# Kernel tuning notes

Measured on AMD Instinct MI355X. Metric: run time of the kernel, lower is better.

Reference implementation:

```python
import jax, jax.numpy as jnp
import numpy as np

L, CH, S = 4096, 512, 64
SAMPLE_RATE = 4096.0


def setup_inputs() -> dict:
    key = jax.random.key(0)
    kx, ka, kc = jax.random.split(key, 3)
    x = jax.random.normal(kx, (L, CH), dtype=jnp.float32)
    # original init: lognegA = log(arange(1..S)) broadcast over channels; any real values work
    lognegA = jnp.broadcast_to(jnp.log(jnp.arange(1, S + 1, dtype=jnp.float32)), (CH, S)) \
        + 0.0 * jax.random.normal(ka, (CH, S), dtype=jnp.float32)
    B = jnp.ones((CH, S), dtype=jnp.float32)
    C = 0.01 * jax.random.normal(kc, (CH, S), dtype=jnp.float32)  # nn.initializers.normal() stddev=0.01
    return {"x": x, "lognegA": lognegA, "B": B, "C": C}


def reference(x, lognegA, B, C):
    length = x.shape[0]
    dt = 1.0 / SAMPLE_RATE
    A = -jnp.exp(lognegA)                         # [C, S], strictly negative
    Bd = (jnp.exp(A * dt) - 1.0) * B / A          # discretized B, [C, S]
    # Vandermonde-style kernel: Ak[l, c, s] = exp(l * A[c, s] * dt)
    Ak = jnp.exp(jnp.einsum('l,cs->lcs', jnp.arange(length, dtype=x.dtype), A * dt))
    K = jnp.einsum('cs,lcs->lc', C * Bd, Ak)      # [L, C] per-channel kernel
    # per-channel full causal convolution, truncated to length
    y = jax.vmap(jnp.convolve, in_axes=1, out_axes=1)(x, K)[:length]
    return y
```

## Files before the change

kernel.cpp:

```cpp
#include <hip/hip_runtime.h>


namespace {

constexpr int L_ = 4096;
constexpr int CH_ = 512;
constexpr int S_ = 64;
constexpr float DT = 1.0f / 4096.0f;
constexpr int SC = S_ * CH_;
constexpr int SG = 16;
constexpr int T_ = 64;
constexpr int NC_ = L_ / T_;
constexpr int GJ = 16;
constexpr int NJ = NC_ / GJ;

__device__ __forceinline__ void params16(const float* __restrict__ la,
                                         const float* __restrict__ Bg,
                                         const float* __restrict__ Cg,
                                         int c, int s0, float* r, float* w) {
  const float4* lap = reinterpret_cast<const float4*>(la + c * S_ + s0);
  if (w == nullptr) {
#pragma unroll
    for (int q = 0; q < 4; ++q) {
      const float4 v = lap[q];
      const float a[4] = {v.x, v.y, v.z, v.w};
#pragma unroll
      for (int t = 0; t < 4; ++t) {
        const float A = -expf(a[t]);
        r[q * 4 + t] = expf(A * DT);
      }
    }
  } else {
    const float4* bp = reinterpret_cast<const float4*>(Bg + c * S_ + s0);
    const float4* cp = reinterpret_cast<const float4*>(Cg + c * S_ + s0);
#pragma unroll
    for (int q = 0; q < 4; ++q) {
      const float4 v = lap[q], bb = bp[q], cc = cp[q];
      const float a[4] = {v.x, v.y, v.z, v.w};
      const float bv[4] = {bb.x, bb.y, bb.z, bb.w};
      const float cv[4] = {cc.x, cc.y, cc.z, cc.w};
#pragma unroll
      for (int t = 0; t < 4; ++t) {
        const float A = -expf(a[t]);
        const float rr = expf(A * DT);
        r[q * 4 + t] = rr;
        w[q * 4 + t] = cv[t] * ((rr - 1.0f) * bv[t] / A);
      }
    }
  }
}

__global__ __launch_bounds__(256)
void k_local(const float* __restrict__ x, const float* __restrict__ la,
             float* __restrict__ E) {
  const int lane = threadIdx.x & 63;
  const int g = threadIdx.x >> 6;
  const int k = blockIdx.x >> 3;
  const int c = ((blockIdx.x & 7) << 6) + lane;
  const int s0 = g * SG;

  const float* xp = x + (size_t)k * T_ * CH_ + c;
  float xb[16];
#pragma unroll
  for (int j = 0; j < 16; ++j) xb[j] = xp[j * CH_];

  float r[SG], h[SG];
  params16(la, nullptr, nullptr, c, s0, r, nullptr);
#pragma unroll
  for (int i = 0; i < SG; ++i) h[i] = 0.0f;

  for (int l0 = 0; l0 < T_; l0 += 16) {
    float xc[16];
#pragma unroll
    for (int j = 0; j < 16; ++j) xc[j] = xb[j];
    const int ln = (l0 + 16 < T_) ? l0 + 16 : l0;
#pragma unroll
    for (int j = 0; j < 16; ++j) xb[j] = xp[(ln + j) * CH_];
#pragma unroll
    for (int j = 0; j < 16; ++j) {
      const float xv = xc[j];
#pragma unroll
      for (int i = 0; i < SG; ++i) h[i] = fmaf(r[i], h[i], xv);
    }
  }

  float* ew = E + (size_t)k * SC + s0 * CH_ + c;
#pragma unroll
  for (int i = 0; i < SG; ++i) ew[i * CH_] = h[i];
}

__global__ __launch_bounds__(256)
void k_comb(const float* __restrict__ la, float* __restrict__ carry) {
  __shared__ float aggs[NJ][64];
  const int p = threadIdx.x & 63;
  const int j = threadIdx.x >> 6;
  const int pid = (blockIdx.x << 6) + p;
  const int s = pid >> 9;
  const int c = pid & (CH_ - 1);

  float v[GJ];
#pragma unroll
  for (int m = 0; m < GJ; ++m) v[m] = carry[(size_t)(j * GJ + m) * SC + pid];

  const float A = -expf(la[c * S_ + s]);
  const float rT = expf(A * (DT * (float)T_));
  float rTG = rT;
  rTG *= rTG;
  rTG *= rTG;
  rTG *= rTG;
  rTG *= rTG;

  float agg = 0.0f;
#pragma unroll
  for (int m = 0; m < GJ; ++m) agg = fmaf(rT, agg, v[m]);
  aggs[j][p] = agg;
  __syncthreads();

  float G = 0.0f;
  for (int j2 = 0; j2 < j; ++j2) G = fmaf(rTG, G, aggs[j2][p]);

  float st = G;
#pragma unroll
  for (int m = 0; m < GJ; ++m) {
    carry[(size_t)(j * GJ + m) * SC + pid] = st;
    st = fmaf(rT, st, v[m]);
  }
}

template <int T, bool USE_CARRY>
__global__ __launch_bounds__(256)
void k_scan(const float* __restrict__ x, const float* __restrict__ la,
            const float* __restrict__ Bg, const float* __restrict__ Cg,
            const float* __restrict__ carry, float* __restrict__ y) {
  __shared__ float lds[4][8][64];

  const int lane = threadIdx.x & 63;
  const int g = threadIdx.x >> 6;
  const int k = blockIdx.x >> 3;
  const int cb = (blockIdx.x & 7) << 6;
  const int c = cb + lane;
  const int s0 = g * SG;

  float h[SG];
  if (USE_CARRY) {
    const float* crd = carry + (size_t)k * SC + s0 * CH_ + c;
#pragma unroll
    for (int i = 0; i < SG; ++i) h[i] = crd[i * CH_];
  } else {
#pragma unroll
    for (int i = 0; i < SG; ++i) h[i] = 0.0f;
  }
  const float* xp = x + (size_t)k * T * CH_ + c;
  float xb[8];
#pragma unroll
  for (int j = 0; j < 8; ++j) xb[j] = xp[j * CH_];

  float r[SG], w[SG];
  params16(la, Bg, Cg, c, s0, r, w);

  float* yp = y + (size_t)k * T * CH_;

  for (int l = 0; l < T; l += 8) {
    float xc[8];
#pragma unroll
    for (int j = 0; j < 8; ++j) xc[j] = xb[j];
    const int ln = (l + 8 < T) ? l + 8 : l;
#pragma unroll
    for (int j = 0; j < 8; ++j) xb[j] = xp[(ln + j) * CH_];

    float part[8];
#pragma unroll
    for (int jj = 0; jj < 8; ++jj) {
      const float xv = xc[jj];
      float a0 = 0, a1 = 0, a2 = 0, a3 = 0;
#pragma unroll
      for (int i = 0; i < SG; i += 4) {
        h[i]     = fmaf(r[i],     h[i],     xv);
        h[i + 1] = fmaf(r[i + 1], h[i + 1], xv);
        h[i + 2] = fmaf(r[i + 2], h[i + 2], xv);
        h[i + 3] = fmaf(r[i + 3], h[i + 3], xv);
        a0 = fmaf(w[i],     h[i],     a0);
        a1 = fmaf(w[i + 1], h[i + 1], a1);
        a2 = fmaf(w[i + 2], h[i + 2], a2);
        a3 = fmaf(w[i + 3], h[i + 3], a3);
      }
      part[jj] = (a0 + a1) + (a2 + a3);
    }

#pragma unroll
    for (int jj = 0; jj < 8; ++jj) lds[g][jj][lane] = part[jj];
    __syncthreads();
#pragma unroll
    for (int p = 0; p < 2; ++p) {
      const int idx = (int)threadIdx.x + p * 256;
      const int jj = idx >> 6;
      const int ln2 = idx & 63;
      const float vv = (lds[0][jj][ln2] + lds[1][jj][ln2]) +
                       (lds[2][jj][ln2] + lds[3][jj][ln2]);
      yp[(size_t)(l + jj) * CH_ + cb + ln2] = vv;
    }
    __syncthreads();
  }
}

}

extern "C" void kernel_launch(void* const* d_in, const int* in_sizes, int n_in,
                              void* d_out, int out_size, void* d_ws, size_t ws_size,
                              hipStream_t stream) {
  const float* x = (const float*)d_in[0];
  const float* la = (const float*)d_in[1];
  const float* B = (const float*)d_in[2];
  const float* C = (const float*)d_in[3];
  float* y = (float*)d_out;
  float* E = (float*)d_ws;

  const size_t need = (size_t)NC_ * SC * sizeof(float);
  if (ws_size >= need) {
    k_local<<<NC_ * 8, 256, 0, stream>>>(x, la, E);
    k_comb<<<SC / 64, 256, 0, stream>>>(la, E);
    k_scan<T_, true><<<NC_ * 8, 256, 0, stream>>>(x, la, B, C, E, y);
  } else {
    k_scan<L_, false><<<8, 256, 0, stream>>>(x, la, B, C, nullptr, y);
  }
}
```

Measured before the change: 90.34 us.

## Fuse three-kernel chunked scan into one persistent kernel with grid barriers

Merges the local-chunk scan, the carry combine and the final output scan into a single kernel launch of 512 blocks, separated by two sharded atomic grid barriers whose counters are zeroed with a memset. The aim is to remove two kernel launch gaps and their inter-kernel drain. In exchange it relies on all 512 blocks being co-resident (launch_bounds 256,2), adds atomic spin-wait costs, and falls back silently after a bounded spin count, which risks incorrect results if residency fails.

After: 186.3 us. +106.3%, slower.

```diff
diff --git a/kernel.cpp b/kernel.cpp
--- a/kernel.cpp
+++ b/kernel.cpp
@@ -12,7 +12,32 @@
 constexpr int T_ = 64;
 constexpr int NC_ = L_ / T_;
 constexpr int GJ = 16;
-constexpr int NJ = NC_ / GJ;
+constexpr int NB = NC_ * 8;
+
+constexpr int CTR_U32 = 25 * 32;
+
+__device__ __forceinline__ void tree_barrier(unsigned* __restrict__ ctr,
+                                             int phase, int shard) {
+  unsigned* sh = ctr + (phase * 16 + shard) * 32;
+  unsigned* rt = ctr + (phase * 16 + 8) * 32;
+  __syncthreads();
+  if (threadIdx.x == 0) {
+    __threadfence();
+    const unsigned t = __hip_atomic_fetch_add(sh, 1u, __ATOMIC_ACQ_REL,
+                                              __HIP_MEMORY_SCOPE_AGENT);
+    if (t == 63u)
+      __hip_atomic_fetch_add(rt, 1u, __ATOMIC_ACQ_REL,
+                             __HIP_MEMORY_SCOPE_AGENT);
+    for (int it = 0; it < 200000; ++it) {
+      if (__hip_atomic_load(rt, __ATOMIC_ACQUIRE,
+                            __HIP_MEMORY_SCOPE_AGENT) >= 8u)
+        break;
+      __builtin_amdgcn_s_sleep(16);
+    }
+    __threadfence();
+  }
+  __syncthreads();
+}
 
 __device__ __forceinline__ void params16(const float* __restrict__ la,
                                          const float* __restrict__ Bg,
@@ -50,128 +75,177 @@
   }
 }
 
-__global__ __launch_bounds__(256)
-void k_local(const float* __restrict__ x, const float* __restrict__ la,
-             float* __restrict__ E) {
+__global__ __launch_bounds__(256, 2)
+void s4d_one(const float* __restrict__ x, const float* __restrict__ la,
+             const float* __restrict__ Bg, const float* __restrict__ Cg,
+             float* __restrict__ carry,
+             unsigned* __restrict__ ctr,
+             float* __restrict__ y) {
+  __shared__ float lds[4][8][64];
+  __shared__ float aggs[4][64];
+
+  const int tid = threadIdx.x;
+  const int bid = blockIdx.x;
+  const int lane = tid & 63;
+  const int g = tid >> 6;
+  const int k = bid >> 3;
+  const int cb = (bid & 7) << 6;
+  const int c = cb + lane;
+  const int s0 = g * SG;
+
+  {
+    const float* xp = x + (size_t)k * T_ * CH_ + c;
+    float xb[16];
+#pragma unroll
+    for (int j = 0; j < 16; ++j) xb[j] = xp[j * CH_];
+
+    float r[SG], h[SG];
+    params16(la, nullptr, nullptr, c, s0, r, nullptr);
+#pragma unroll
+    for (int i = 0; i < SG; ++i) h[i] = 0.0f;
+
+    for (int l0 = 0; l0 < T_; l0 += 16) {
+      float xc[16];
+#pragma unroll
+      for (int j = 0; j < 16; ++j) xc[j] = xb[j];
+      const int ln = (l0 + 16 < T_) ? l0 + 16 : l0;
+#pragma unroll
+      for (int j = 0; j < 16; ++j) xb[j] = xp[(ln + j) * CH_];
+#pragma unroll
+      for (int j = 0; j < 16; ++j) {
+        const float xv = xc[j];
+#pragma unroll
+        for (int i = 0; i < SG; ++i) h[i] = fmaf(r[i], h[i], xv);
+      }
+    }
+
+    float* ew = carry + (size_t)k * SC + s0 * CH_ + c;
+#pragma unroll
+    for (int i = 0; i < SG; ++i) ew[i * CH_] = h[i];
+  }
+
+  tree_barrier(ctr, 0, bid & 7);
+
+  {
+    const int p = tid & 63;
+    const int j = g;
+    const int pid = (bid << 6) + p;
+    const int s = pid >> 9;
+    const int c2 = pid & (CH_ - 1);
+
+    float v[GJ];
+#pragma unroll
+    for (int m = 0; m < GJ; ++m) v[m] = carry[(size_t)(j * GJ + m) * SC + pid];
+
+    const float A = -expf(la[c2 * S_ + s]);
+    const float rT = expf(A * (DT * (float)T_));
+    float rTG = rT;
+    rTG *= rTG; rTG *= rTG; rTG *= rTG; rTG *= rTG;
+
+    float agg = 0.0f;
+#pragma unroll
+    for (int m = 0; m < GJ; ++m) agg = fmaf(rT, agg, v[m]);
+    aggs[j][p] = agg;
+    __syncthreads();
+
+    float G = 0.0f;
+    for (int j2 = 0; j2 < j; ++j2) G = fmaf(rTG, G, aggs[j2][p]);
+
+    float st = G;
+#pragma unroll
+    for (int m = 0; m < GJ; ++m) {
+      carry[(size_t)(j * GJ + m) * SC + pid] = st;
+      st = fmaf(rT, st, v[m]);
+    }
+  }
+
+  tree_barrier(ctr, 1, bid & 7);
+
+  {
+    float h[SG];
+    const float* crd = carry + (size_t)k * SC + s0 * CH_ + c;
+#pragma unroll
+    for (int i = 0; i < SG; ++i) h[i] = crd[i * CH_];
+
+    const float* xp = x + (size_t)k * T_ * CH_ + c;
+    float xb[8];
+#pragma unroll
+    for (int j = 0; j < 8; ++j) xb[j] = xp[j * CH_];
+
+    float r[SG], w[SG];
+    params16(la, Bg, Cg, c, s0, r, w);
+
+    float* yp = y + (size_t)k * T_ * CH_;
+
+    for (int l = 0; l < T_; l += 8) {
+      float xc[8];
+#pragma unroll
+      for (int j = 0; j < 8; ++j) xc[j] = xb[j];
+      const int ln = (l + 8 < T_) ? l + 8 : l;
+#pragma unroll
+      for (int j = 0; j < 8; ++j) xb[j] = xp[(ln + j) * CH_];
+
+      float part[8];
+#pragma unroll
+      for (int jj = 0; jj < 8; ++jj) {
+        const float xv = xc[jj];
+        float a0 = 0, a1 = 0, a2 = 0, a3 = 0;
+#pragma unroll
+        for (int i = 0; i < SG; i += 4) {
+          h[i]     = fmaf(r[i],     h[i],     xv);
+          h[i + 1] = fmaf(r[i + 1], h[i + 1], xv);
+          h[i + 2] = fmaf(r[i + 2], h[i + 2], xv);
+          h[i + 3] = fmaf(r[i + 3], h[i + 3], xv);
+          a0 = fmaf(w[i],     h[i],     a0);
+          a1 = fmaf(w[i + 1], h[i + 1], a1);
+          a2 = fmaf(w[i + 2], h[i + 2], a2);
+          a3 = fmaf(w[i + 3], h[i + 3], a3);
+        }
+        part[jj] = (a0 + a1) + (a2 + a3);
+      }
+
+#pragma unroll
+      for (int jj = 0; jj < 8; ++jj) lds[g][jj][lane] = part[jj];
+      __syncthreads();
+#pragma unroll
+      for (int p = 0; p < 2; ++p) {
+        const int idx = tid + p * 256;
+        const int jj = idx >> 6;
+        const int ln2 = idx & 63;
+        const float vv = (lds[0][jj][ln2] + lds[1][jj][ln2]) +
+                         (lds[2][jj][ln2] + lds[3][jj][ln2]);
+        yp[(size_t)(l + jj) * CH_ + cb + ln2] = vv;
+      }
+      __syncthreads();
+    }
+  }
+}
+
+__global__ __launch_bounds__(256) void k_scan_full(const float* __restrict__ x,
+                                                   const float* __restrict__ la,
+                                                   const float* __restrict__ Bg,
+                                                   const float* __restrict__ Cg,
+                                                   float* __restrict__ y) {
+  __shared__ float lds[4][8][64];
   const int lane = threadIdx.x & 63;
   const int g = threadIdx.x >> 6;
-  const int k = blockIdx.x >> 3;
-  const int c = ((blockIdx.x & 7) << 6) + lane;
-  const int s0 = g * SG;
-
-  const float* xp = x + (size_t)k * T_ * CH_ + c;
-  float xb[16];
-#pragma unroll
-  for (int j = 0; j < 16; ++j) xb[j] = xp[j * CH_];
-
-  float r[SG], h[SG];
-  params16(la, nullptr, nullptr, c, s0, r, nullptr);
-#pragma unroll
-  for (int i = 0; i < SG; ++i) h[i] = 0.0f;
-
-  for (int l0 = 0; l0 < T_; l0 += 16) {
-    float xc[16];
-#pragma unroll
-    for (int j = 0; j < 16; ++j) xc[j] = xb[j];
-    const int ln = (l0 + 16 < T_) ? l0 + 16 : l0;
-#pragma unroll
-    for (int j = 0; j < 16; ++j) xb[j] = xp[(ln + j) * CH_];
-#pragma unroll
-    for (int j = 0; j < 16; ++j) {
-      const float xv = xc[j];
-#pragma unroll
-      for (int i = 0; i < SG; ++i) h[i] = fmaf(r[i], h[i], xv);
-    }
-  }
-
-  float* ew = E + (size_t)k * SC + s0 * CH_ + c;
-#pragma unroll
-  for (int i = 0; i < SG; ++i) ew[i * CH_] = h[i];
-}
-
-__global__ __launch_bounds__(256)
-void k_comb(const float* __restrict__ la, float* __restrict__ carry) {
-  __shared__ float aggs[NJ][64];
-  const int p = threadIdx.x & 63;
-  const int j = threadIdx.x >> 6;
-  const int pid = (blockIdx.x << 6) + p;
-  const int s = pid >> 9;
-  const int c = pid & (CH_ - 1);
-
-  float v[GJ];
-#pragma unroll
-  for (int m = 0; m < GJ; ++m) v[m] = carry[(size_t)(j * GJ + m) * SC + pid];
-
-  const float A = -expf(la[c * S_ + s]);
-  const float rT = expf(A * (DT * (float)T_));
-  float rTG = rT;
-  rTG *= rTG;
-  rTG *= rTG;
-  rTG *= rTG;
-  rTG *= rTG;
-
-  float agg = 0.0f;
-#pragma unroll
-  for (int m = 0; m < GJ; ++m) agg = fmaf(rT, agg, v[m]);
-  aggs[j][p] = agg;
-  __syncthreads();
-
-  float G = 0.0f;
-  for (int j2 = 0; j2 < j; ++j2) G = fmaf(rTG, G, aggs[j2][p]);
-
-  float st = G;
-#pragma unroll
-  for (int m = 0; m < GJ; ++m) {
-    carry[(size_t)(j * GJ + m) * SC + pid] = st;
-    st = fmaf(rT, st, v[m]);
-  }
-}
-
-template <int T, bool USE_CARRY>
-__global__ __launch_bounds__(256)
-void k_scan(const float* __restrict__ x, const float* __restrict__ la,
-            const float* __restrict__ Bg, const float* __restrict__ Cg,
-            const float* __restrict__ carry, float* __restrict__ y) {
-  __shared__ float lds[4][8][64];
-
-  const int lane = threadIdx.x & 63;
-  const int g = threadIdx.x >> 6;
-  const int k = blockIdx.x >> 3;
   const int cb = (blockIdx.x & 7) << 6;
   const int c = cb + lane;
   const int s0 = g * SG;
 
-  float h[SG];
-  if (USE_CARRY) {
-    const float* crd = carry + (size_t)k * SC + s0 * CH_ + c;
-#pragma unroll
-    for (int i = 0; i < SG; ++i) h[i] = crd[i * CH_];
-  } else {
-#pragma unroll
-    for (int i = 0; i < SG; ++i) h[i] = 0.0f;
-  }
-  const float* xp = x + (size_t)k * T * CH_ + c;
-  float xb[8];
-#pragma unroll
-  for (int j = 0; j < 8; ++j) xb[j] = xp[j * CH_];
-
-  float r[SG], w[SG];
+  float r[SG], w[SG], h[SG];
   params16(la, Bg, Cg, c, s0, r, w);
-
-  float* yp = y + (size_t)k * T * CH_;
-
-  for (int l = 0; l < T; l += 8) {
-    float xc[8];
-#pragma unroll
-    for (int j = 0; j < 8; ++j) xc[j] = xb[j];
-    const int ln = (l + 8 < T) ? l + 8 : l;
-#pragma unroll
-    for (int j = 0; j < 8; ++j) xb[j] = xp[(ln + j) * CH_];
-
+#pragma unroll
+  for (int i = 0; i < SG; ++i) h[i] = 0.0f;
+
+  const float* xp = x + c;
+  float* yp = y;
+
+  for (int l = 0; l < L_; l += 8) {
     float part[8];
 #pragma unroll
     for (int jj = 0; jj < 8; ++jj) {
-      const float xv = xc[jj];
+      const float xv = xp[(size_t)(l + jj) * CH_];
       float a0 = 0, a1 = 0, a2 = 0, a3 = 0;
 #pragma unroll
       for (int i = 0; i < SG; i += 4) {
@@ -186,7 +260,6 @@
       }
       part[jj] = (a0 + a1) + (a2 + a3);
     }
-
 #pragma unroll
     for (int jj = 0; jj < 8; ++jj) lds[g][jj][lane] = part[jj];
     __syncthreads();
@@ -194,10 +267,10 @@
     for (int p = 0; p < 2; ++p) {
       const int idx = (int)threadIdx.x + p * 256;
       const int jj = idx >> 6;
-      const int ln2 = idx & 63;
-      const float vv = (lds[0][jj][ln2] + lds[1][jj][ln2]) +
-                       (lds[2][jj][ln2] + lds[3][jj][ln2]);
-      yp[(size_t)(l + jj) * CH_ + cb + ln2] = vv;
+      const int ln = idx & 63;
+      const float vv = (lds[0][jj][ln] + lds[1][jj][ln]) +
+                       (lds[2][jj][ln] + lds[3][jj][ln]);
+      yp[(size_t)(l + jj) * CH_ + cb + ln] = vv;
     }
     __syncthreads();
   }
@@ -213,14 +286,16 @@
   const float* B = (const float*)d_in[2];
   const float* C = (const float*)d_in[3];
   float* y = (float*)d_out;
-  float* E = (float*)d_ws;
-
-  const size_t need = (size_t)NC_ * SC * sizeof(float);
+  float* ws = (float*)d_ws;
+
+  const size_t carry_f = (size_t)NC_ * SC;
+  const size_t need = carry_f * sizeof(float) + CTR_U32 * sizeof(unsigned);
   if (ws_size >= need) {
-    k_local<<<NC_ * 8, 256, 0, stream>>>(x, la, E);
-    k_comb<<<SC / 64, 256, 0, stream>>>(la, E);
-    k_scan<T_, true><<<NC_ * 8, 256, 0, stream>>>(x, la, B, C, E, y);
+    float* carry = ws;
+    unsigned* ctr = (unsigned*)(ws + carry_f);
+    hipMemsetAsync((void*)ctr, 0, CTR_U32 * sizeof(unsigned), stream);
+    s4d_one<<<NB, 256, 0, stream>>>(x, la, B, C, carry, ctr, y);
   } else {
-    k_scan<L_, false><<<8, 256, 0, stream>>>(x, la, B, C, nullptr, y);
-  }
-}
+    k_scan_full<<<8, 256, 0, stream>>>(x, la, B, C, y);
+  }
+}
```
